# Kernel optimization log

Measured on AMD Instinct MI355X. Metric: run time of the kernel, lower is better.

## Reference

```python
import jax, jax.numpy as jnp
import numpy as np

N_NODES = 100000


def _add_self_loops(edge_index, n):
    loop = jnp.arange(n, dtype=edge_index.dtype)
    src = jnp.concatenate([edge_index[0], loop])
    dst = jnp.concatenate([edge_index[1], loop])
    return src, dst


def _gcn_conv(x, W, b, src, dst, n):
    # h = X W, then symmetric-normalized scatter-add over edges (PyG GCNConv)
    h = x @ W
    ones = jnp.ones(src.shape[0], dtype=h.dtype)
    deg = jax.ops.segment_sum(ones, dst, num_segments=n)  # in-degree incl. self loops
    dinv = jnp.where(deg > 0, jax.lax.rsqrt(deg), 0.0)
    norm = dinv[src] * dinv[dst]                           # [E]
    msg = h[src] * norm[:, None]                           # gather + scale
    out = jax.ops.segment_sum(msg, dst, num_segments=n)    # scatter-add
    return out + b


def setup_inputs() -> dict:
    key = jax.random.key(0)
    k1, k2, k3, k4 = jax.random.split(key, 4)
    F, H, C = 128, 128, 16
    x = jax.random.normal(k1, (N_NODES, F), dtype=jnp.float32)
    edge_index = jax.random.randint(k2, (2, 1600000), 0, N_NODES, dtype=jnp.int64)
    W1 = jax.random.normal(k3, (F, H), dtype=jnp.float32) / np.sqrt(F)
    b1 = jnp.zeros((H,), dtype=jnp.float32)
    W2 = jax.random.normal(k4, (H, C), dtype=jnp.float32) / np.sqrt(H)
    b2 = jnp.zeros((C,), dtype=jnp.float32)
    return {"x": x, "edge_index": edge_index, "W1": W1, "b1": b1, "W2": W2, "b2": b2}


def reference(x, edge_index, W1, b1, W2, b2):
    n = x.shape[0]
    src, dst = _add_self_loops(edge_index, n)
    h = _gcn_conv(x, W1, b1, src, dst, n)
    h = jax.nn.relu(h)
    # dropout(p=0.1) treated as identity (deterministic eval-mode reference)
    logits = _gcn_conv(h, W2, b2, src, dst, n)
    return logits, jax.nn.log_softmax(logits, axis=1)
```

## Files before the change

### kernel.cpp

```cpp
#include <hip/hip_runtime.h>
#include <math.h>


#define ELLW 72

typedef __attribute__((ext_vector_type(8))) short short8;
typedef __attribute__((ext_vector_type(4))) float f32x4;

__device__ __forceinline__ float bf2f(unsigned short u) {
    return __uint_as_float(((unsigned int)u) << 16);
}
__device__ __forceinline__ unsigned short f2bf(float f) {
    unsigned int u = __float_as_uint(f);
    unsigned int r = (u + 0x7fffu + ((u >> 16) & 1u)) >> 16;
    return (unsigned short)r;
}

__global__ void k_prep(int* __restrict__ deg, unsigned short* __restrict__ h,
                       float* __restrict__ g, int4* __restrict__ col4,
                       const float* __restrict__ W1, unsigned short* __restrict__ wt,
                       int n, int colsz4) {
    int i = blockIdx.x * blockDim.x + threadIdx.x;
    if (i < n) deg[i] = 0;
    if (i < colsz4) col4[i] = make_int4(n, n, n, n);
    if (i < 16384) {
        int nc = i >> 7, k = i & 127;
        wt[i] = f2bf(W1[k * 128 + nc]);
    }
    if (blockIdx.x == 0) {
        int t = threadIdx.x;
        if (t < 128) h[(size_t)n * 128 + t] = 0;
        if (t < 16) g[(size_t)n * 16 + t] = 0.f;
    }
}

__global__ void k_build(const int* __restrict__ src, const int* __restrict__ dst, int E,
                        int* __restrict__ deg, int* __restrict__ col) {
    int e = blockIdx.x * blockDim.x + threadIdx.x;
    if (e < E) {
        int d = dst[e];
        int p = atomicAdd(&deg[d], 1);
        if (p < ELLW) col[(size_t)d * ELLW + p] = src[e];
    }
}

__global__ void k_gemm1(const float* __restrict__ x, const unsigned short* __restrict__ wt,
                        const int* __restrict__ deg, unsigned short* __restrict__ h,
                        int n) {
    __shared__ unsigned short xs[64 * 136];
    const int t = threadIdx.x;
    const int row0 = blockIdx.x * 64;
    for (int i = t; i < 2048; i += 256) {
        int r = i >> 5, c4 = (i & 31) << 2;
        int gr = row0 + r;
        float4 v = make_float4(0.f, 0.f, 0.f, 0.f);
        if (gr < n) v = *(const float4*)(x + (size_t)gr * 128 + c4);
        ushort4 u;
        u.x = f2bf(v.x); u.y = f2bf(v.y); u.z = f2bf(v.z); u.w = f2bf(v.w);
        *(ushort4*)(xs + r * 136 + c4) = u;
    }
    __syncthreads();
    const int w = t >> 6;
    const int lane = t & 63;
    const int m = lane & 15, q = lane >> 4;
    f32x4 acc[8];
#pragma unroll
    for (int ns = 0; ns < 8; ++ns) acc[ns] = (f32x4){0.f, 0.f, 0.f, 0.f};
#pragma unroll
    for (int kt = 0; kt < 4; ++kt) {
        short8 a = *(const short8*)(xs + (w * 16 + m) * 136 + kt * 32 + q * 8);
#pragma unroll
        for (int ns = 0; ns < 8; ++ns) {
            short8 b = *(const short8*)((const short*)wt + (ns * 16 + m) * 128 + kt * 32 + q * 8);
            acc[ns] = __builtin_amdgcn_mfma_f32_16x16x32_bf16(a, b, acc[ns], 0, 0, 0);
        }
    }
    unsigned short* xsw = xs + (w * 16) * 136;
    float srow[4];
#pragma unroll
    for (int reg = 0; reg < 4; ++reg) {
        int gr = row0 + w * 16 + q * 4 + reg;
        srow[reg] = (gr < n) ? rsqrtf((float)(deg[gr] + 1)) : 0.f;
    }
#pragma unroll
    for (int ns = 0; ns < 8; ++ns)
#pragma unroll
        for (int reg = 0; reg < 4; ++reg)
            xsw[(q * 4 + reg) * 136 + ns * 16 + m] = f2bf(acc[ns][reg] * srow[reg]);
    __syncthreads();
#pragma unroll
    for (int it = 0; it < 8; ++it) {
        int rl = (lane >> 5) + it * 2;
        int off = (lane & 31) * 4;
        int gr = row0 + w * 16 + rl;
        if (gr < n)
            *(ushort4*)(h + (size_t)gr * 128 + off) = *(const ushort4*)(xsw + rl * 136 + off);
    }
}

__global__ __launch_bounds__(256, 2) void k_gather1f(
        const unsigned short* __restrict__ h, const int* __restrict__ deg,
        const int* __restrict__ col, const float* __restrict__ b1,
        const float* __restrict__ W2, float* __restrict__ g, int n) {
    const int t = threadIdx.x;
    const int lane = t & 15;
    const int d = blockIdx.x * 16 + (t >> 4);
    if (d >= n) return;
    int dg = deg[d];
    if (dg > ELLW) dg = ELLW;
    const float dd = rsqrtf((float)(dg + 1));
    const int kend = (dg + 7) & ~7;
    const int* ecol = col + (size_t)d * ELLW;

    float aA[8], aB[8];
    {
        short8 u = *(const short8*)(h + (size_t)d * 128 + lane * 8);
#pragma unroll
        for (int j = 0; j < 8; ++j) {
            aA[j] = bf2f((unsigned short)u[j]);
            aB[j] = 0.f;
        }
    }
    for (int k = 0; k < kend; k += 8) {
        int4 c0 = *(const int4*)(ecol + k);
        int4 c1 = *(const int4*)(ecol + k + 4);
        short8 u0 = *(const short8*)(h + (size_t)c0.x * 128 + lane * 8);
        short8 u1 = *(const short8*)(h + (size_t)c0.y * 128 + lane * 8);
        short8 u2 = *(const short8*)(h + (size_t)c0.z * 128 + lane * 8);
        short8 u3 = *(const short8*)(h + (size_t)c0.w * 128 + lane * 8);
        short8 u4 = *(const short8*)(h + (size_t)c1.x * 128 + lane * 8);
        short8 u5 = *(const short8*)(h + (size_t)c1.y * 128 + lane * 8);
        short8 u6 = *(const short8*)(h + (size_t)c1.z * 128 + lane * 8);
        short8 u7 = *(const short8*)(h + (size_t)c1.w * 128 + lane * 8);
#pragma unroll
        for (int j = 0; j < 8; ++j) {
            aA[j] += bf2f((unsigned short)u0[j]) + bf2f((unsigned short)u2[j]) +
                     bf2f((unsigned short)u4[j]) + bf2f((unsigned short)u6[j]);
            aB[j] += bf2f((unsigned short)u1[j]) + bf2f((unsigned short)u3[j]) +
                     bf2f((unsigned short)u5[j]) + bf2f((unsigned short)u7[j]);
        }
    }
    float y[8];
    const float* b1p = b1 + lane * 8;
#pragma unroll
    for (int j = 0; j < 8; ++j)
        y[j] = fmaxf(fmaf(aA[j] + aB[j], dd, b1p[j]), 0.f);
    const float4* w2v = (const float4*)(W2 + lane * 8 * 16);
    float4 z0 = make_float4(0.f, 0.f, 0.f, 0.f);
    float4 z1 = z0, z2 = z0, z3 = z0;
#pragma unroll
    for (int j = 0; j < 8; ++j) {
        float4 w0 = w2v[j * 4 + 0], w1 = w2v[j * 4 + 1];
        float4 w2 = w2v[j * 4 + 2], w3 = w2v[j * 4 + 3];
        float yj = y[j];
        z0.x = fmaf(yj, w0.x, z0.x); z0.y = fmaf(yj, w0.y, z0.y);
        z0.z = fmaf(yj, w0.z, z0.z); z0.w = fmaf(yj, w0.w, z0.w);
        z1.x = fmaf(yj, w1.x, z1.x); z1.y = fmaf(yj, w1.y, z1.y);
        z1.z = fmaf(yj, w1.z, z1.z); z1.w = fmaf(yj, w1.w, z1.w);
        z2.x = fmaf(yj, w2.x, z2.x); z2.y = fmaf(yj, w2.y, z2.y);
        z2.z = fmaf(yj, w2.z, z2.z); z2.w = fmaf(yj, w2.w, z2.w);
        z3.x = fmaf(yj, w3.x, z3.x); z3.y = fmaf(yj, w3.y, z3.y);
        z3.z = fmaf(yj, w3.z, z3.z); z3.w = fmaf(yj, w3.w, z3.w);
    }
#pragma unroll
    for (int mm = 1; mm < 16; mm <<= 1) {
        z0.x += __shfl_xor(z0.x, mm); z0.y += __shfl_xor(z0.y, mm);
        z0.z += __shfl_xor(z0.z, mm); z0.w += __shfl_xor(z0.w, mm);
        z1.x += __shfl_xor(z1.x, mm); z1.y += __shfl_xor(z1.y, mm);
        z1.z += __shfl_xor(z1.z, mm); z1.w += __shfl_xor(z1.w, mm);
        z2.x += __shfl_xor(z2.x, mm); z2.y += __shfl_xor(z2.y, mm);
        z2.z += __shfl_xor(z2.z, mm); z2.w += __shfl_xor(z2.w, mm);
        z3.x += __shfl_xor(z3.x, mm); z3.y += __shfl_xor(z3.y, mm);
        z3.z += __shfl_xor(z3.z, mm); z3.w += __shfl_xor(z3.w, mm);
    }
    if (lane < 4) {
        float4 z = (lane == 0) ? z0 : (lane == 1) ? z1 : (lane == 2) ? z2 : z3;
        z.x *= dd; z.y *= dd; z.z *= dd; z.w *= dd;
        *(float4*)(g + (size_t)d * 16 + lane * 4) = z;
    }
}

#define FACC(acc, v) \
    acc.x += v.x; acc.y += v.y; acc.z += v.z; acc.w += v.w

__global__ void k_gather2(const float* __restrict__ g, const int* __restrict__ deg,
                          const int* __restrict__ col, const float* __restrict__ b2,
                          float* __restrict__ out, int n) {
    const int t = threadIdx.x;
    const int d = blockIdx.x * 64 + (t >> 2);
    if (d >= n) return;
    const int l = t & 3;
    int dg = deg[d];
    if (dg > ELLW) dg = ELLW;
    const float dd = rsqrtf((float)(dg + 1));
    const int kend = (dg + 7) & ~7;
    const int* ecol = col + (size_t)d * ELLW;

    float4 aA = *(const float4*)(g + (size_t)d * 16 + l * 4);
    float4 aB = make_float4(0.f, 0.f, 0.f, 0.f);
    float4 aC = aB, aD = aB;
    for (int k = 0; k < kend; k += 8) {
        int4 c0 = *(const int4*)(ecol + k);
        int4 c1 = *(const int4*)(ecol + k + 4);
        float4 h0 = *(const float4*)(g + (size_t)c0.x * 16 + l * 4);
        float4 h1 = *(const float4*)(g + (size_t)c0.y * 16 + l * 4);
        float4 h2 = *(const float4*)(g + (size_t)c0.z * 16 + l * 4);
        float4 h3 = *(const float4*)(g + (size_t)c0.w * 16 + l * 4);
        float4 h4 = *(const float4*)(g + (size_t)c1.x * 16 + l * 4);
        float4 h5 = *(const float4*)(g + (size_t)c1.y * 16 + l * 4);
        float4 h6 = *(const float4*)(g + (size_t)c1.z * 16 + l * 4);
        float4 h7 = *(const float4*)(g + (size_t)c1.w * 16 + l * 4);
        FACC(aA, h0); FACC(aB, h1); FACC(aC, h2); FACC(aD, h3);
        FACC(aA, h4); FACC(aB, h5); FACC(aC, h6); FACC(aD, h7);
    }
    float4 bv = *(const float4*)(b2 + l * 4);
    float4 acc;
    acc.x = fmaf(aA.x + aB.x + aC.x + aD.x, dd, bv.x);
    acc.y = fmaf(aA.y + aB.y + aC.y + aD.y, dd, bv.y);
    acc.z = fmaf(aA.z + aB.z + aC.z + aD.z, dd, bv.z);
    acc.w = fmaf(aA.w + aB.w + aC.w + aD.w, dd, bv.w);
    *(float4*)(out + (size_t)d * 16 + l * 4) = acc;
    float m = fmaxf(fmaxf(acc.x, acc.y), fmaxf(acc.z, acc.w));
    m = fmaxf(m, __shfl_xor(m, 1));
    m = fmaxf(m, __shfl_xor(m, 2));
    float e = expf(acc.x - m) + expf(acc.y - m) + expf(acc.z - m) + expf(acc.w - m);
    e += __shfl_xor(e, 1);
    e += __shfl_xor(e, 2);
    float ls = m + logf(e);
    float4 o;
    o.x = acc.x - ls; o.y = acc.y - ls; o.z = acc.z - ls; o.w = acc.w - ls;
    *(float4*)(out + (size_t)n * 16 + (size_t)d * 16 + l * 4) = o;
}

static inline size_t align256(size_t v) { return (v + 255) & ~(size_t)255; }

extern "C" void kernel_launch(void* const* d_in, const int* in_sizes, int n_in,
                              void* d_out, int out_size, void* d_ws, size_t ws_size,
                              hipStream_t stream) {
    const float* x  = (const float*)d_in[0];
    const int*   ei = (const int*)d_in[1];
    const float* W1 = (const float*)d_in[2];
    const float* b1 = (const float*)d_in[3];
    const float* W2 = (const float*)d_in[4];
    const float* b2 = (const float*)d_in[5];
    float* out = (float*)d_out;

    const int n = in_sizes[0] / 128;
    const int E = in_sizes[1] / 2;
    const int* src = ei;
    const int* dst = ei + E;
    const int COLSZ = n * ELLW;
    const int COLSZ4 = COLSZ / 4;

    char* base = (char*)d_ws;
    size_t off = 0;
    int* deg = (int*)(base + off); off = align256(off + (size_t)n * 4);
    int* col = (int*)(base + off); off = align256(off + (size_t)COLSZ * 4);
    unsigned short* wt = (unsigned short*)(base + off); off = align256(off + 128 * 128 * 2);
    unsigned short* h = (unsigned short*)(base + off); off = align256(off + ((size_t)n + 1) * 128 * 2);
    float* g = (float*)(base + off); off = align256(off + ((size_t)n + 1) * 16 * 4);

    {
        int prep_items = COLSZ4;
        k_prep<<<(prep_items + 255) / 256, 256, 0, stream>>>(deg, h, g, (int4*)col, W1, wt, n, COLSZ4);
    }
    k_build<<<(E + 255) / 256, 256, 0, stream>>>(src, dst, E, deg, col);

    k_gemm1<<<(n + 63) / 64, 256, 0, stream>>>(x, wt, deg, h, n);
    k_gather1f<<<(n + 15) / 16, 256, 0, stream>>>(h, deg, col, b1, W2, g, n);

    k_gather2<<<(n + 63) / 64, 256, 0, stream>>>(g, deg, col, b2, out, n);
}
```

Baseline: 399.1 us.

## Build ELL adjacency via bucketed counting sort with shared-memory atomics

Replaces the global-atomic ELL build with a two-pass bucketed binning: a per-block histogram of destination buckets, a single-block scan, a binning pass that packs source and local destination into one int, and a per-bucket kernel that fills ELL rows using shared-memory degree counters. It also drops the full memset of the column array and pads only each row's tail up to a multiple of 8 with the sentinel. The aim is to avoid contended global atomics, scattered writes and the large fill pass, at the cost of more kernel launches, an extra E-sized buffer and a serial scan. The packing assumes node ids fit in 17 bits and that block and bucket counts fit the fixed maxima. Downstream kernels must also never read column slots past each row's padded length.

```diff
diff --git a/kernel.cpp b/kernel.cpp
--- a/kernel.cpp
+++ b/kernel.cpp
@@ -3,6 +3,10 @@
 
 
 #define ELLW 72
+#define EPB 16384
+#define BSH 9
+#define MAXEB 100
+#define MAXBK 200
 
 typedef __attribute__((ext_vector_type(8))) short short8;
 typedef __attribute__((ext_vector_type(4))) float f32x4;
@@ -16,31 +20,108 @@
     return (unsigned short)r;
 }
 
-__global__ void k_prep(int* __restrict__ deg, unsigned short* __restrict__ h,
-                       float* __restrict__ g, int4* __restrict__ col4,
+__global__ void k_prep(unsigned short* __restrict__ h, float* __restrict__ g,
                        const float* __restrict__ W1, unsigned short* __restrict__ wt,
-                       int n, int colsz4) {
+                       int n) {
     int i = blockIdx.x * blockDim.x + threadIdx.x;
-    if (i < n) deg[i] = 0;
-    if (i < colsz4) col4[i] = make_int4(n, n, n, n);
     if (i < 16384) {
         int nc = i >> 7, k = i & 127;
         wt[i] = f2bf(W1[k * 128 + nc]);
     }
-    if (blockIdx.x == 0) {
-        int t = threadIdx.x;
-        if (t < 128) h[(size_t)n * 128 + t] = 0;
-        if (t < 16) g[(size_t)n * 16 + t] = 0.f;
-    }
-}
-
-__global__ void k_build(const int* __restrict__ src, const int* __restrict__ dst, int E,
-                        int* __restrict__ deg, int* __restrict__ col) {
-    int e = blockIdx.x * blockDim.x + threadIdx.x;
-    if (e < E) {
+    if (i < 128) h[(size_t)n * 128 + i] = 0;
+    if (i < 16) g[(size_t)n * 16 + i] = 0.f;
+}
+
+__global__ void k_hist(const int* __restrict__ dst, int E,
+                       int* __restrict__ hist, int nbuck) {
+    __shared__ int lh[MAXBK];
+    const int t = threadIdx.x, blk = blockIdx.x;
+    for (int i = t; i < nbuck; i += 256) lh[i] = 0;
+    __syncthreads();
+    const int e0 = blk * EPB;
+    const int e1 = min(e0 + EPB, E);
+    for (int e = e0 + t; e < e1; e += 256)
+        atomicAdd(&lh[dst[e] >> BSH], 1);
+    __syncthreads();
+    for (int i = t; i < nbuck; i += 256)
+        hist[blk * nbuck + i] = lh[i];
+}
+
+__global__ void k_scan(int* __restrict__ hist, int* __restrict__ bstart,
+                       int* __restrict__ bcount, int neb, int nbuck) {
+    __shared__ unsigned short lh[MAXEB * MAXBK];
+    __shared__ int sc[256];
+    const int t = threadIdx.x;
+    const int items = neb * nbuck;
+    for (int i = t; i < items; i += 256) lh[i] = (unsigned short)hist[i];
+    __syncthreads();
+    int total = 0;
+    if (t < nbuck)
+        for (int blk = 0; blk < neb; ++blk) total += lh[blk * nbuck + t];
+    sc[t] = total;
+    __syncthreads();
+    for (int o = 1; o < 256; o <<= 1) {
+        int x = 0;
+        if (t >= o) x = sc[t - o];
+        __syncthreads();
+        if (t >= o) sc[t] += x;
+        __syncthreads();
+    }
+    if (t < nbuck) {
+        int run = sc[t] - total;
+        bstart[t] = run;
+        bcount[t] = total;
+        for (int blk = 0; blk < neb; ++blk) {
+            int idx = blk * nbuck + t;
+            int v = lh[idx];
+            hist[idx] = run;
+            run += v;
+        }
+    }
+}
+
+__global__ void k_bin(const int* __restrict__ src, const int* __restrict__ dst, int E,
+                      const int* __restrict__ hist, int* __restrict__ binned, int nbuck) {
+    __shared__ int cnt[MAXBK];
+    const int t = threadIdx.x, blk = blockIdx.x;
+    for (int i = t; i < nbuck; i += 256) cnt[i] = hist[blk * nbuck + i];
+    __syncthreads();
+    const int e0 = blk * EPB;
+    const int e1 = min(e0 + EPB, E);
+    for (int e = e0 + t; e < e1; e += 256) {
         int d = dst[e];
-        int p = atomicAdd(&deg[d], 1);
-        if (p < ELLW) col[(size_t)d * ELLW + p] = src[e];
+        int b = d >> BSH;
+        int pos = atomicAdd(&cnt[b], 1);
+        binned[pos] = src[e] | ((d & ((1 << BSH) - 1)) << 17);
+    }
+}
+
+__global__ void k_ell(const int* __restrict__ binned, const int* __restrict__ bstart,
+                      const int* __restrict__ bcount, int* __restrict__ deg,
+                      int* __restrict__ col, int n) {
+    __shared__ int ldeg[1 << BSH];
+    const int t = threadIdx.x, b = blockIdx.x;
+    const int node0 = b << BSH;
+    for (int i = t; i < (1 << BSH); i += 256) ldeg[i] = 0;
+    __syncthreads();
+    const int st = bstart[b], cv = bcount[b];
+    for (int i = t; i < cv; i += 256) {
+        int v = binned[st + i];
+        int s = v & 0x1FFFF;
+        int dl = v >> 17;
+        int q = atomicAdd(&ldeg[dl], 1);
+        if (q < ELLW) col[(size_t)(node0 + dl) * ELLW + q] = s;
+    }
+    __syncthreads();
+    for (int i = t; i < (1 << BSH); i += 256) {
+        int node = node0 + i;
+        if (node < n) {
+            int dgv = ldeg[i];
+            deg[node] = dgv;
+            int dc = dgv > ELLW ? ELLW : dgv;
+            int kend = (dc + 7) & ~7;
+            for (int q = dc; q < kend; ++q) col[(size_t)node * ELLW + q] = n;
+        }
     }
 }
 
@@ -249,22 +330,26 @@
     const int E = in_sizes[1] / 2;
     const int* src = ei;
     const int* dst = ei + E;
-    const int COLSZ = n * ELLW;
-    const int COLSZ4 = COLSZ / 4;
+    const int NEB = (E + EPB - 1) / EPB;
+    const int NBUCK = (n + (1 << BSH) - 1) >> BSH;
 
     char* base = (char*)d_ws;
     size_t off = 0;
     int* deg = (int*)(base + off); off = align256(off + (size_t)n * 4);
-    int* col = (int*)(base + off); off = align256(off + (size_t)COLSZ * 4);
+    int* col = (int*)(base + off); off = align256(off + (size_t)n * ELLW * 4);
     unsigned short* wt = (unsigned short*)(base + off); off = align256(off + 128 * 128 * 2);
     unsigned short* h = (unsigned short*)(base + off); off = align256(off + ((size_t)n + 1) * 128 * 2);
     float* g = (float*)(base + off); off = align256(off + ((size_t)n + 1) * 16 * 4);
-
-    {
-        int prep_items = COLSZ4;
-        k_prep<<<(prep_items + 255) / 256, 256, 0, stream>>>(deg, h, g, (int4*)col, W1, wt, n, COLSZ4);
-    }
-    k_build<<<(E + 255) / 256, 256, 0, stream>>>(src, dst, E, deg, col);
+    int* hist = (int*)(base + off); off = align256(off + (size_t)MAXEB * MAXBK * 4);
+    int* bstart = (int*)(base + off); off = align256(off + (size_t)MAXBK * 4);
+    int* bcount = (int*)(base + off); off = align256(off + (size_t)MAXBK * 4);
+    int* binned = (int*)(base + off); off = align256(off + (size_t)E * 4);
+
+    k_prep<<<64, 256, 0, stream>>>(h, g, W1, wt, n);
+    k_hist<<<NEB, 256, 0, stream>>>(dst, E, hist, NBUCK);
+    k_scan<<<1, 256, 0, stream>>>(hist, bstart, bcount, NEB, NBUCK);
+    k_bin<<<NEB, 256, 0, stream>>>(src, dst, E, hist, binned, NBUCK);
+    k_ell<<<NBUCK, 256, 0, stream>>>(binned, bstart, bcount, deg, col, n);
 
     k_gemm1<<<(n + 63) / 64, 256, 0, stream>>>(x, wt, deg, h, n);
     k_gather1f<<<(n + 15) / 16, 256, 0, stream>>>(h, deg, col, b1, W2, g, n);
```

Measured after the change: 360.2 us. -9.8%, faster.
